# Performance work log

Measured on AMD Instinct MI355X. Metric: run time of the kernel, lower is better.

Reference implementation:

```python
import jax, jax.numpy as jnp
import numpy as np

B, F, D, L, N = 2048, 40, 64, 3, 40  # batch, num_fields, embed_dim, num_layers, num_subspaces


def setup_inputs() -> dict:
    key = jax.random.key(0)
    inputs = jax.random.normal(key, (B, F, D), dtype=jnp.float32)
    # Parameters per layer, matching torch init exactly:
    #   W     = identity(D) repeated over out_subspaces -> [N, D, D]
    #   alpha = ones([num_fields, in_subspaces, out_subspaces]); in_subspaces == F for
    #           layer 0 and == N afterwards; with N == F all layers share shape [F, N, N]
    #   h     = ones([N, D, 1])
    W = jnp.broadcast_to(jnp.eye(D, dtype=jnp.float32), (L, N, D, D)).copy()
    alpha = jnp.ones((L, F, N, N), dtype=jnp.float32)
    h = jnp.ones((L, N, D, 1), dtype=jnp.float32)
    return {"inputs": inputs, "W": W, "alpha": alpha, "h": h}


def _fusion_layer(B0, Bi, W, alpha, h):
    # Original math: fusion[b,n,D,d] = sum_{f,i} alpha[f,i,n] * B0[b,f,D] * Bi[b,i,d]
    #                out[b,n,D]     = sum_d fusion[b,n,D,d] * W[n,D,d] * h[n,d]
    # Reordered to avoid the [b,f,n,D,d] outer-product tensor:
    M = W * h[:, :, 0][:, None, :]                 # [n, D, d] = W * h broadcast over D
    C = jnp.einsum('bid,nDd->binD', Bi, M)         # contract embed dim d first
    out = jnp.einsum('bfD,fin,binD->bnD', B0, alpha, C)
    return out


def reference(inputs, W, alpha, h):
    B_i = inputs
    for l in range(L):
        B_i = _fusion_layer(inputs, B_i, W[l], alpha[l], h[l])
    return B_i
```

## Files before the change

kernel.cpp:

```cpp
#include <hip/hip_runtime.h>


typedef __bf16 bf16x8 __attribute__((ext_vector_type(8)));
typedef float  f32x16 __attribute__((ext_vector_type(16)));
typedef unsigned short us4 __attribute__((ext_vector_type(4)));

constexpr int BATCH = 2048;
constexpr int FDIM  = 40;
constexpr int DDIM  = 64;
constexpr int LAY   = 3;
constexpr int IPAD  = 64;
constexpr int FPAD  = 48;
constexpr int NSPL  = 4;
constexpr int NPB   = FDIM / NSPL;

__device__ __forceinline__ unsigned short f2bf(float f) {
  union { float f; unsigned u; } v; v.f = f;
  unsigned r = v.u + 0x7fff + ((v.u >> 16) & 1);
  return (unsigned short)(r >> 16);
}

__global__ __launch_bounds__(256) void prep_all(
    const float* __restrict__ inputs, const float* __restrict__ W,
    const float* __restrict__ h, const float* __restrict__ alpha,
    unsigned short* __restrict__ B0b, unsigned short* __restrict__ B0T,
    unsigned short* __restrict__ M, unsigned short* __restrict__ AT) {
  __shared__ float lds[FDIM][DDIM + 1];
  if (blockIdx.x < BATCH) {
    const int b = blockIdx.x;
    const float* src = inputs + (size_t)b * FDIM * DDIM;
    for (int cch = threadIdx.x; cch < FDIM * DDIM / 4; cch += 256) {
      float4 v = reinterpret_cast<const float4*>(src)[cch];
      int e = cch * 4;
      int f = e >> 6, d = e & 63;
      lds[f][d] = v.x; lds[f][d + 1] = v.y; lds[f][d + 2] = v.z; lds[f][d + 3] = v.w;
      us4 o = { f2bf(v.x), f2bf(v.y), f2bf(v.z), f2bf(v.w) };
      reinterpret_cast<us4*>(B0b + (size_t)b * FDIM * DDIM)[cch] = o;
    }
    __syncthreads();
    for (int cch = threadIdx.x; cch < DDIM * FPAD / 4; cch += 256) {
      int f4 = cch % (FPAD / 4);
      int d  = cch / (FPAD / 4);
      us4 o = {0, 0, 0, 0};
      if (f4 < FDIM / 4) {
        int f = f4 * 4;
        o[0] = f2bf(lds[f][d]);     o[1] = f2bf(lds[f + 1][d]);
        o[2] = f2bf(lds[f + 2][d]); o[3] = f2bf(lds[f + 3][d]);
      }
      reinterpret_cast<us4*>(B0T + (size_t)b * DDIM * FPAD)[cch] = o;
    }
    return;
  }
  int j = (blockIdx.x - BATCH) * 256 + threadIdx.x;
  const int nM4 = LAY * FDIM * DDIM * DDIM / 4;
  const int nA4 = LAY * FDIM * IPAD * FPAD / 4;
  if (j < nM4) {
    int e  = j * 4;
    int d  = e & 63;
    int ln = e >> 12;
    float4 wv = *reinterpret_cast<const float4*>(W + e);
    float4 hv = *reinterpret_cast<const float4*>(h + ln * DDIM + d);
    us4 o = { f2bf(wv.x * hv.x), f2bf(wv.y * hv.y), f2bf(wv.z * hv.z), f2bf(wv.w * hv.w) };
    *reinterpret_cast<us4*>(M + e) = o;
    return;
  }
  j -= nM4;
  if (j >= nA4) return;
  {
    int e  = j * 4;
    int f  = e % FPAD;
    int ii = (e / FPAD) % IPAD;
    int n  = (e / (FPAD * IPAD)) % FDIM;
    int l  = e / (FPAD * IPAD * FDIM);
    us4 o = {0, 0, 0, 0};
    if (ii < FDIM) {
#pragma unroll
      for (int k = 0; k < 4; ++k)
        if (f + k < FDIM)
          o[k] = f2bf(alpha[(((size_t)l * FDIM + f + k) * FDIM + ii) * FDIM + n]);
    }
    *reinterpret_cast<us4*>(AT + e) = o;
  }
}

template <bool FINAL>
__global__ __launch_bounds__(128, 2) void layer_k(
    const unsigned short* __restrict__ Bi,
    const unsigned short* __restrict__ B0T,
    const unsigned short* __restrict__ Mt,
    const unsigned short* __restrict__ ATt,
    void* __restrict__ outp)
{
  const int tid  = threadIdx.x;
  const int lane = tid & 63;
  const int w    = tid >> 6;
  const int c    = lane & 31;
  const int h    = lane >> 5;
  const int bg   = blockIdx.x >> 2;
  const int nBase = (blockIdx.x & 3) * NPB;
  const int bb   = bg * 4 + w * 2;

  bf16x8 aBi[2][2][4];
#pragma unroll
  for (int b2 = 0; b2 < 2; ++b2)
#pragma unroll
    for (int it = 0; it < 2; ++it) {
      int row = it * 32 + c; if (row > FDIM - 1) row = FDIM - 1;
#pragma unroll
      for (int ks = 0; ks < 4; ++ks)
        aBi[b2][it][ks] = *reinterpret_cast<const bf16x8*>(
            Bi + ((size_t)(bb + b2) * FDIM + row) * DDIM + ks * 16 + h * 8);
    }

  bf16x8 bT[2][2][3];
#pragma unroll
  for (int b2 = 0; b2 < 2; ++b2)
#pragma unroll
    for (int dt = 0; dt < 2; ++dt)
#pragma unroll
      for (int ks = 0; ks < 3; ++ks)
        bT[b2][dt][ks] = *reinterpret_cast<const bf16x8*>(
            B0T + ((size_t)(bb + b2) * DDIM + dt * 32 + c) * FPAD + ks * 16 + h * 8);

  for (int ln = 0; ln < NPB; ++ln) {
    const int n = nBase + ln;
    const unsigned short* Mn = Mt  + n * (DDIM * DDIM);
    const unsigned short* An = ATt + n * (IPAD * FPAD);

    bf16x8 mb[2][4];
#pragma unroll
    for (int dt = 0; dt < 2; ++dt)
#pragma unroll
      for (int ks = 0; ks < 4; ++ks)
        mb[dt][ks] = *reinterpret_cast<const bf16x8*>(
            Mn + (dt * 32 + c) * DDIM + ks * 16 + h * 8);

    bf16x8 at[2][3];
#pragma unroll
    for (int it = 0; it < 2; ++it)
#pragma unroll
      for (int ks = 0; ks < 3; ++ks)
        at[it][ks] = *reinterpret_cast<const bf16x8*>(
            An + (it * 32 + c) * FPAD + ks * 16 + h * 8);

    float pout[2][2] = {{0.f, 0.f}, {0.f, 0.f}};

#pragma unroll
    for (int it = 0; it < 2; ++it) {
#pragma unroll
      for (int dt = 0; dt < 2; ++dt) {
        f32x16 aC0 = {0,0,0,0,0,0,0,0,0,0,0,0,0,0,0,0};
        f32x16 aC1 = {0,0,0,0,0,0,0,0,0,0,0,0,0,0,0,0};
        f32x16 aR0 = {0,0,0,0,0,0,0,0,0,0,0,0,0,0,0,0};
        f32x16 aR1 = {0,0,0,0,0,0,0,0,0,0,0,0,0,0,0,0};
        __builtin_amdgcn_s_setprio(1);
#pragma unroll
        for (int ks = 0; ks < 3; ++ks) {
          aC0 = __builtin_amdgcn_mfma_f32_32x32x16_bf16(aBi[0][it][ks], mb[dt][ks], aC0, 0, 0, 0);
          aC1 = __builtin_amdgcn_mfma_f32_32x32x16_bf16(aBi[1][it][ks], mb[dt][ks], aC1, 0, 0, 0);
          aR0 = __builtin_amdgcn_mfma_f32_32x32x16_bf16(at[it][ks], bT[0][dt][ks], aR0, 0, 0, 0);
          aR1 = __builtin_amdgcn_mfma_f32_32x32x16_bf16(at[it][ks], bT[1][dt][ks], aR1, 0, 0, 0);
        }
        aC0 = __builtin_amdgcn_mfma_f32_32x32x16_bf16(aBi[0][it][3], mb[dt][3], aC0, 0, 0, 0);
        aC1 = __builtin_amdgcn_mfma_f32_32x32x16_bf16(aBi[1][it][3], mb[dt][3], aC1, 0, 0, 0);
        __builtin_amdgcn_s_setprio(0);
        {
          float t0 = 0.f, t1 = 0.f, t2 = 0.f, t3 = 0.f;
#pragma unroll
          for (int r = 0; r < 4; ++r) {
            t0 += aC0[r] * aR0[r];         t1 += aC0[r + 4] * aR0[r + 4];
            t2 += aC0[r + 8] * aR0[r + 8]; t3 += aC0[r + 12] * aR0[r + 12];
          }
          pout[0][dt] += (t0 + t1) + (t2 + t3);
        }
        {
          float t0 = 0.f, t1 = 0.f, t2 = 0.f, t3 = 0.f;
#pragma unroll
          for (int r = 0; r < 4; ++r) {
            t0 += aC1[r] * aR1[r];         t1 += aC1[r + 4] * aR1[r + 4];
            t2 += aC1[r + 8] * aR1[r + 8]; t3 += aC1[r + 12] * aR1[r + 12];
          }
          pout[1][dt] += (t0 + t1) + (t2 + t3);
        }
      }
    }

#pragma unroll
    for (int b2 = 0; b2 < 2; ++b2) {
      float v0 = pout[b2][0] + __shfl_xor(pout[b2][0], 32, 64);
      float v1 = pout[b2][1] + __shfl_xor(pout[b2][1], 32, 64);
      float val = h ? v1 : v0;
      size_t off = ((size_t)(bb + b2) * FDIM + n) * DDIM + lane;
      if (FINAL) ((float*)outp)[off] = val;
      else       ((unsigned short*)outp)[off] = f2bf(val);
    }
  }
}

extern "C" void kernel_launch(void* const* d_in, const int* in_sizes, int n_in,
                              void* d_out, int out_size, void* d_ws, size_t ws_size,
                              hipStream_t stream) {
  const float* inputs = (const float*)d_in[0];
  const float* W      = (const float*)d_in[1];
  const float* alpha  = (const float*)d_in[2];
  const float* h      = (const float*)d_in[3];

  char* ws = (char*)d_ws;
  const size_t S   = (size_t)BATCH * FDIM * DDIM * 2;
  const size_t ST  = (size_t)BATCH * DDIM * FPAD * 2;
  unsigned short* Bi1 = (unsigned short*)(ws);
  unsigned short* Bi2 = (unsigned short*)(ws + S);
  unsigned short* B0b = (unsigned short*)(ws + 2 * S);
  unsigned short* B0T = (unsigned short*)(ws + 3 * S);
  unsigned short* Mb  = (unsigned short*)(ws + 3 * S + ST);
  unsigned short* ATb = (unsigned short*)(ws + 3 * S + ST + (size_t)LAY * FDIM * DDIM * DDIM * 2);

  const int nPrep4 = (LAY * FDIM * DDIM * DDIM + LAY * FDIM * IPAD * FPAD) / 4;
  const int prepBlocks = BATCH + (nPrep4 + 255) / 256;
  prep_all<<<prepBlocks, 256, 0, stream>>>(inputs, W, h, alpha, B0b, B0T, Mb, ATb);

  dim3 grid(BATCH / 4 * NSPL), blk(128);
  const size_t mL = (size_t)FDIM * DDIM * DDIM;
  const size_t aL = (size_t)FDIM * IPAD * FPAD;
  layer_k<false><<<grid, blk, 0, stream>>>(B0b, B0T, Mb, ATb, Bi1);
  layer_k<false><<<grid, blk, 0, stream>>>(Bi1, B0T, Mb + mL, ATb + aL, Bi2);
  layer_k<true ><<<grid, blk, 0, stream>>>(Bi2, B0T, Mb + 2 * mL, ATb + 2 * aL, d_out);
}
```

Measured before the change: 261.6 us.

## Stage per-subspace M and alpha tiles in LDS shared across 8 waves

Each block now has 512 threads and covers 16 batch rows instead of 4. The W*h and alpha tiles for each pair of subspaces are loaded cooperatively into double-buffered LDS, with an XOR swizzle on M, instead of every wave reading them from global memory. Staging the next chunk is interleaved with compute, and block indices are remapped so neighbouring subspace splits land together. The MFMA loop is also split per batch to lower register pressure. This adds a barrier per chunk and about 60KB of LDS per block, and the grid shrinks to 512 blocks, which may limit latency hiding.

```diff
diff --git a/kernel.cpp b/kernel.cpp
--- a/kernel.cpp
+++ b/kernel.cpp
@@ -13,6 +13,8 @@
 constexpr int FPAD  = 48;
 constexpr int NSPL  = 4;
 constexpr int NPB   = FDIM / NSPL;
+constexpr int BPB   = 16;
+constexpr int NCH   = NPB / 2;
 
 __device__ __forceinline__ unsigned short f2bf(float f) {
   union { float f; unsigned u; } v; v.f = f;
@@ -84,21 +86,27 @@
 }
 
 template <bool FINAL>
-__global__ __launch_bounds__(128, 2) void layer_k(
+__global__ __launch_bounds__(512, 2) void layer_k(
     const unsigned short* __restrict__ Bi,
     const unsigned short* __restrict__ B0T,
     const unsigned short* __restrict__ Mt,
     const unsigned short* __restrict__ ATt,
     void* __restrict__ outp)
 {
+  __shared__ unsigned short smM[2][2][64 * 64];
+  __shared__ unsigned short smA[2][2][64 * 56];
+
   const int tid  = threadIdx.x;
   const int lane = tid & 63;
   const int w    = tid >> 6;
   const int c    = lane & 31;
   const int h    = lane >> 5;
-  const int bg   = blockIdx.x >> 2;
-  const int nBase = (blockIdx.x & 3) * NPB;
-  const int bb   = bg * 4 + w * 2;
+
+  const int L  = (blockIdx.x & 7) * 64 + (blockIdx.x >> 3);
+  const int bg = L >> 2;
+  const int ns = L & 3;
+  const int nBase = ns * NPB;
+  const int bb = bg * BPB + w * 2;
 
   bf16x8 aBi[2][2][4];
 #pragma unroll
@@ -111,7 +119,6 @@
         aBi[b2][it][ks] = *reinterpret_cast<const bf16x8*>(
             Bi + ((size_t)(bb + b2) * FDIM + row) * DDIM + ks * 16 + h * 8);
     }
-
   bf16x8 bT[2][2][3];
 #pragma unroll
   for (int b2 = 0; b2 < 2; ++b2)
@@ -122,69 +129,93 @@
         bT[b2][dt][ks] = *reinterpret_cast<const bf16x8*>(
             B0T + ((size_t)(bb + b2) * DDIM + dt * 32 + c) * FPAD + ks * 16 + h * 8);
 
-  for (int ln = 0; ln < NPB; ++ln) {
-    const int n = nBase + ln;
-    const unsigned short* Mn = Mt  + n * (DDIM * DDIM);
-    const unsigned short* An = ATt + n * (IPAD * FPAD);
-
-    bf16x8 mb[2][4];
+  auto stageL = [&](int cc, bf16x8 (&sM)[2], bf16x8 (&sA)[2]) {
+#pragma unroll
+    for (int r = 0; r < 2; ++r) {
+      int k = tid + r * 512;
+      int nn = k >> 9, rem = k & 511;
+      int row = rem >> 3, c8 = rem & 7;
+      sM[r] = *reinterpret_cast<const bf16x8*>(
+          Mt + (size_t)(nBase + cc * 2 + nn) * (DDIM * DDIM) + row * 64 + c8 * 8);
+    }
+#pragma unroll
+    for (int r = 0; r < 2; ++r) {
+      int k = tid + r * 512;
+      if (k < 768) {
+        int nn = k / 384, rem = k % 384;
+        int row = rem / 6, c6 = rem % 6;
+        sA[r] = *reinterpret_cast<const bf16x8*>(
+            ATt + (size_t)(nBase + cc * 2 + nn) * (IPAD * FPAD) + row * 48 + c6 * 8);
+      }
+    }
+  };
+  auto stageW = [&](int cc, const bf16x8 (&sM)[2], const bf16x8 (&sA)[2]) {
+    int bs = cc & 1;
+#pragma unroll
+    for (int r = 0; r < 2; ++r) {
+      int k = tid + r * 512;
+      int nn = k >> 9, rem = k & 511;
+      int row = rem >> 3, c8 = rem & 7;
+      *reinterpret_cast<bf16x8*>(
+          &smM[bs][nn][row * 64 + ((c8 ^ (row & 7)) * 8)]) = sM[r];
+    }
+#pragma unroll
+    for (int r = 0; r < 2; ++r) {
+      int k = tid + r * 512;
+      if (k < 768) {
+        int nn = k / 384, rem = k % 384;
+        int row = rem / 6, c6 = rem % 6;
+        *reinterpret_cast<bf16x8*>(&smA[bs][nn][row * 56 + c6 * 8]) = sA[r];
+      }
+    }
+  };
+
+  auto compute = [&](int nl, int bs) {
+    const int n  = nBase + nl;
+    const int nn = nl & 1;
+    const unsigned short* mL = &smM[bs][nn][0];
+    const unsigned short* aL = &smA[bs][nn][0];
+    bf16x8 mb[2][4], at[2][3];
 #pragma unroll
     for (int dt = 0; dt < 2; ++dt)
 #pragma unroll
       for (int ks = 0; ks < 4; ++ks)
         mb[dt][ks] = *reinterpret_cast<const bf16x8*>(
-            Mn + (dt * 32 + c) * DDIM + ks * 16 + h * 8);
-
-    bf16x8 at[2][3];
+            mL + (dt * 32 + c) * 64 + (((ks * 2 + h) ^ (c & 7)) * 8));
 #pragma unroll
     for (int it = 0; it < 2; ++it)
 #pragma unroll
       for (int ks = 0; ks < 3; ++ks)
         at[it][ks] = *reinterpret_cast<const bf16x8*>(
-            An + (it * 32 + c) * FPAD + ks * 16 + h * 8);
+            aL + (it * 32 + c) * 56 + (ks * 2 + h) * 8);
 
     float pout[2][2] = {{0.f, 0.f}, {0.f, 0.f}};
-
 #pragma unroll
     for (int it = 0; it < 2; ++it) {
 #pragma unroll
       for (int dt = 0; dt < 2; ++dt) {
-        f32x16 aC0 = {0,0,0,0,0,0,0,0,0,0,0,0,0,0,0,0};
-        f32x16 aC1 = {0,0,0,0,0,0,0,0,0,0,0,0,0,0,0,0};
-        f32x16 aR0 = {0,0,0,0,0,0,0,0,0,0,0,0,0,0,0,0};
-        f32x16 aR1 = {0,0,0,0,0,0,0,0,0,0,0,0,0,0,0,0};
-        __builtin_amdgcn_s_setprio(1);
-#pragma unroll
-        for (int ks = 0; ks < 3; ++ks) {
-          aC0 = __builtin_amdgcn_mfma_f32_32x32x16_bf16(aBi[0][it][ks], mb[dt][ks], aC0, 0, 0, 0);
-          aC1 = __builtin_amdgcn_mfma_f32_32x32x16_bf16(aBi[1][it][ks], mb[dt][ks], aC1, 0, 0, 0);
-          aR0 = __builtin_amdgcn_mfma_f32_32x32x16_bf16(at[it][ks], bT[0][dt][ks], aR0, 0, 0, 0);
-          aR1 = __builtin_amdgcn_mfma_f32_32x32x16_bf16(at[it][ks], bT[1][dt][ks], aR1, 0, 0, 0);
+#pragma unroll
+        for (int b2 = 0; b2 < 2; ++b2) {
+          f32x16 aC = {0,0,0,0,0,0,0,0,0,0,0,0,0,0,0,0};
+          f32x16 aR = {0,0,0,0,0,0,0,0,0,0,0,0,0,0,0,0};
+          __builtin_amdgcn_s_setprio(1);
+#pragma unroll
+          for (int ks = 0; ks < 3; ++ks) {
+            aC = __builtin_amdgcn_mfma_f32_32x32x16_bf16(aBi[b2][it][ks], mb[dt][ks], aC, 0, 0, 0);
+            aR = __builtin_amdgcn_mfma_f32_32x32x16_bf16(at[it][ks], bT[b2][dt][ks], aR, 0, 0, 0);
+          }
+          aC = __builtin_amdgcn_mfma_f32_32x32x16_bf16(aBi[b2][it][3], mb[dt][3], aC, 0, 0, 0);
+          __builtin_amdgcn_s_setprio(0);
+          float t0 = 0.f, t1 = 0.f, t2 = 0.f, t3 = 0.f;
+#pragma unroll
+          for (int r = 0; r < 4; ++r) {
+            t0 += aC[r] * aR[r];         t1 += aC[r + 4] * aR[r + 4];
+            t2 += aC[r + 8] * aR[r + 8]; t3 += aC[r + 12] * aR[r + 12];
+          }
+          pout[b2][dt] += (t0 + t1) + (t2 + t3);
         }
-        aC0 = __builtin_amdgcn_mfma_f32_32x32x16_bf16(aBi[0][it][3], mb[dt][3], aC0, 0, 0, 0);
-        aC1 = __builtin_amdgcn_mfma_f32_32x32x16_bf16(aBi[1][it][3], mb[dt][3], aC1, 0, 0, 0);
-        __builtin_amdgcn_s_setprio(0);
-        {
-          float t0 = 0.f, t1 = 0.f, t2 = 0.f, t3 = 0.f;
-#pragma unroll
-          for (int r = 0; r < 4; ++r) {
-            t0 += aC0[r] * aR0[r];         t1 += aC0[r + 4] * aR0[r + 4];
-            t2 += aC0[r + 8] * aR0[r + 8]; t3 += aC0[r + 12] * aR0[r + 12];
-          }
-          pout[0][dt] += (t0 + t1) + (t2 + t3);
-        }
-        {
-          float t0 = 0.f, t1 = 0.f, t2 = 0.f, t3 = 0.f;
-#pragma unroll
-          for (int r = 0; r < 4; ++r) {
-            t0 += aC1[r] * aR1[r];         t1 += aC1[r + 4] * aR1[r + 4];
-            t2 += aC1[r + 8] * aR1[r + 8]; t3 += aC1[r + 12] * aR1[r + 12];
-          }
-          pout[1][dt] += (t0 + t1) + (t2 + t3);
-        }
-      }
-    }
-
+      }
+    }
 #pragma unroll
     for (int b2 = 0; b2 < 2; ++b2) {
       float v0 = pout[b2][0] + __shfl_xor(pout[b2][0], 32, 64);
@@ -194,6 +225,24 @@
       if (FINAL) ((float*)outp)[off] = val;
       else       ((unsigned short*)outp)[off] = f2bf(val);
     }
+  };
+
+  {
+    bf16x8 sM[2], sA[2];
+    stageL(0, sM, sA);
+    stageW(0, sM, sA);
+  }
+  __syncthreads();
+#pragma unroll 1
+  for (int cc = 0; cc < NCH; ++cc) {
+    const int bs = cc & 1;
+    const int nf = w & 1;
+    bf16x8 sM[2], sA[2];
+    if (cc + 1 < NCH) stageL(cc + 1, sM, sA);
+    compute(cc * 2 + nf, bs);
+    if (cc + 1 < NCH) stageW(cc + 1, sM, sA);
+    compute(cc * 2 + (nf ^ 1), bs);
+    __syncthreads();
   }
 }
 
@@ -219,7 +268,7 @@
   const int prepBlocks = BATCH + (nPrep4 + 255) / 256;
   prep_all<<<prepBlocks, 256, 0, stream>>>(inputs, W, h, alpha, B0b, B0T, Mb, ATb);
 
-  dim3 grid(BATCH / 4 * NSPL), blk(128);
+  dim3 grid(BATCH / BPB * NSPL), blk(512);
   const size_t mL = (size_t)FDIM * DDIM * DDIM;
   const size_t aL = (size_t)FDIM * IPAD * FPAD;
   layer_k<false><<<grid, blk, 0, stream>>>(B0b, B0T, Mb, ATb, Bi1);
```

After: 235.0 us. -10.2%, faster.

## Stage per-subspace M and alpha slabs in LDS via double-buffered async DMA

Applied to the files above, without the earlier changes.

Each per-n M and alpha-transpose slab is now loaded cooperatively into double-buffered shared memory with global_load_lds, so 4 waves (8 batch rows) share one load instead of each wave re-reading from global/L2. The M slab gets an XOR swizzle applied in prep to avoid LDS bank conflicts, the alpha slab uses a 56-element row pitch, the block grows to 256 threads, and the block index is remapped to group neighbouring blocks. The MFMA loop is also reordered to keep only two accumulators live at a time, cutting register pressure. In exchange there is a block-wide barrier per n and added LDS use, which may limit occupancy.

```diff
diff --git a/kernel.cpp b/kernel.cpp
--- a/kernel.cpp
+++ b/kernel.cpp
@@ -9,15 +9,24 @@
 constexpr int FDIM  = 40;
 constexpr int DDIM  = 64;
 constexpr int LAY   = 3;
-constexpr int IPAD  = 64;
 constexpr int FPAD  = 48;
+constexpr int APAD  = 56;
 constexpr int NSPL  = 4;
 constexpr int NPB   = FDIM / NSPL;
+constexpr int BPB   = 8;
+constexpr int MSLAB = DDIM * DDIM;
+constexpr int ASLAB = DDIM * APAD;
 
 __device__ __forceinline__ unsigned short f2bf(float f) {
   union { float f; unsigned u; } v; v.f = f;
   unsigned r = v.u + 0x7fff + ((v.u >> 16) & 1);
   return (unsigned short)(r >> 16);
+}
+
+__device__ __forceinline__ void dma16(unsigned short* lds, const unsigned short* g) {
+  __builtin_amdgcn_global_load_lds(
+      (const __attribute__((address_space(1))) unsigned int*)g,
+      (__attribute__((address_space(3))) unsigned int*)lds, 16, 0, 0);
 }
 
 __global__ __launch_bounds__(256) void prep_all(
@@ -52,26 +61,29 @@
     return;
   }
   int j = (blockIdx.x - BATCH) * 256 + threadIdx.x;
-  const int nM4 = LAY * FDIM * DDIM * DDIM / 4;
-  const int nA4 = LAY * FDIM * IPAD * FPAD / 4;
+  const int nM4 = LAY * FDIM * MSLAB / 4;
+  const int nA4 = LAY * FDIM * ASLAB / 4;
   if (j < nM4) {
-    int e  = j * 4;
-    int d  = e & 63;
-    int ln = e >> 12;
-    float4 wv = *reinterpret_cast<const float4*>(W + e);
-    float4 hv = *reinterpret_cast<const float4*>(h + ln * DDIM + d);
-    us4 o = { f2bf(wv.x * hv.x), f2bf(wv.y * hv.y), f2bf(wv.z * hv.z), f2bf(wv.w * hv.w) };
-    *reinterpret_cast<us4*>(M + e) = o;
+    int e   = j * 4;
+    int ln  = e >> 12;
+    int row = (e >> 6) & 63;
+    int jc  = (e >> 3) & 7;
+    int o   = e & 7;
+    int ds  = ((jc ^ (row & 7)) << 3) + o;
+    float4 wv = *reinterpret_cast<const float4*>(W + ((size_t)ln * 64 + row) * 64 + ds);
+    float4 hv = *reinterpret_cast<const float4*>(h + (size_t)ln * 64 + ds);
+    us4 ov = { f2bf(wv.x * hv.x), f2bf(wv.y * hv.y), f2bf(wv.z * hv.z), f2bf(wv.w * hv.w) };
+    *reinterpret_cast<us4*>(M + e) = ov;
     return;
   }
   j -= nM4;
   if (j >= nA4) return;
   {
     int e  = j * 4;
-    int f  = e % FPAD;
-    int ii = (e / FPAD) % IPAD;
-    int n  = (e / (FPAD * IPAD)) % FDIM;
-    int l  = e / (FPAD * IPAD * FDIM);
+    int f  = e % APAD;
+    int ii = (e / APAD) & 63;
+    int n  = (e / ASLAB) % FDIM;
+    int l  = e / (ASLAB * FDIM);
     us4 o = {0, 0, 0, 0};
     if (ii < FDIM) {
 #pragma unroll
@@ -84,21 +96,27 @@
 }
 
 template <bool FINAL>
-__global__ __launch_bounds__(128, 2) void layer_k(
+__global__ __launch_bounds__(256, 4) void layer_k(
     const unsigned short* __restrict__ Bi,
     const unsigned short* __restrict__ B0T,
     const unsigned short* __restrict__ Mt,
     const unsigned short* __restrict__ ATt,
     void* __restrict__ outp)
 {
+  __shared__ unsigned short smM[2][MSLAB];
+  __shared__ unsigned short smA[2][ASLAB];
+
   const int tid  = threadIdx.x;
   const int lane = tid & 63;
   const int w    = tid >> 6;
   const int c    = lane & 31;
   const int h    = lane >> 5;
-  const int bg   = blockIdx.x >> 2;
-  const int nBase = (blockIdx.x & 3) * NPB;
-  const int bb   = bg * 4 + w * 2;
+
+  const int L  = (blockIdx.x & 7) * 128 + (blockIdx.x >> 3);
+  const int bg = L >> 2;
+  const int ns = L & 3;
+  const int nBase = ns * NPB;
+  const int bb = bg * BPB + w * 2;
 
   bf16x8 aBi[2][2][4];
 #pragma unroll
@@ -111,7 +129,6 @@
         aBi[b2][it][ks] = *reinterpret_cast<const bf16x8*>(
             Bi + ((size_t)(bb + b2) * FDIM + row) * DDIM + ks * 16 + h * 8);
     }
-
   bf16x8 bT[2][2][3];
 #pragma unroll
   for (int b2 = 0; b2 < 2; ++b2)
@@ -122,69 +139,65 @@
         bT[b2][dt][ks] = *reinterpret_cast<const bf16x8*>(
             B0T + ((size_t)(bb + b2) * DDIM + dt * 32 + c) * FPAD + ks * 16 + h * 8);
 
-  for (int ln = 0; ln < NPB; ++ln) {
-    const int n = nBase + ln;
-    const unsigned short* Mn = Mt  + n * (DDIM * DDIM);
-    const unsigned short* An = ATt + n * (IPAD * FPAD);
-
-    bf16x8 mb[2][4];
+  const f32x16 z16 = {0,0,0,0,0,0,0,0,0,0,0,0,0,0,0,0};
+
+  auto dmaChunk = [&](int nl, int bs) {
+    const unsigned short* Ms = Mt  + (size_t)(nBase + nl) * MSLAB;
+    const unsigned short* As = ATt + (size_t)(nBase + nl) * ASLAB;
+#pragma unroll
+    for (int r = 0; r < 2; ++r) {
+      int k = tid + r * 256;
+      dma16(&smM[bs][k * 8], Ms + k * 8);
+    }
+    dma16(&smA[bs][tid * 8], As + tid * 8);
+    if (tid < 192) dma16(&smA[bs][(tid + 256) * 8], As + (tid + 256) * 8);
+  };
+
+  auto compute = [&](int nl, int bs) {
+    const int n = nBase + nl;
+    const unsigned short* mL = &smM[bs][0];
+    const unsigned short* aL = &smA[bs][0];
+    bf16x8 mb[2][4], at[2][3];
 #pragma unroll
     for (int dt = 0; dt < 2; ++dt)
 #pragma unroll
       for (int ks = 0; ks < 4; ++ks)
         mb[dt][ks] = *reinterpret_cast<const bf16x8*>(
-            Mn + (dt * 32 + c) * DDIM + ks * 16 + h * 8);
-
-    bf16x8 at[2][3];
+            mL + (dt * 32 + c) * 64 + (((ks * 2 + h) ^ (c & 7)) * 8));
 #pragma unroll
     for (int it = 0; it < 2; ++it)
 #pragma unroll
       for (int ks = 0; ks < 3; ++ks)
         at[it][ks] = *reinterpret_cast<const bf16x8*>(
-            An + (it * 32 + c) * FPAD + ks * 16 + h * 8);
+            aL + (it * 32 + c) * APAD + (ks * 2 + h) * 8);
 
     float pout[2][2] = {{0.f, 0.f}, {0.f, 0.f}};
-
 #pragma unroll
     for (int it = 0; it < 2; ++it) {
 #pragma unroll
       for (int dt = 0; dt < 2; ++dt) {
-        f32x16 aC0 = {0,0,0,0,0,0,0,0,0,0,0,0,0,0,0,0};
-        f32x16 aC1 = {0,0,0,0,0,0,0,0,0,0,0,0,0,0,0,0};
-        f32x16 aR0 = {0,0,0,0,0,0,0,0,0,0,0,0,0,0,0,0};
-        f32x16 aR1 = {0,0,0,0,0,0,0,0,0,0,0,0,0,0,0,0};
-        __builtin_amdgcn_s_setprio(1);
-#pragma unroll
-        for (int ks = 0; ks < 3; ++ks) {
-          aC0 = __builtin_amdgcn_mfma_f32_32x32x16_bf16(aBi[0][it][ks], mb[dt][ks], aC0, 0, 0, 0);
-          aC1 = __builtin_amdgcn_mfma_f32_32x32x16_bf16(aBi[1][it][ks], mb[dt][ks], aC1, 0, 0, 0);
-          aR0 = __builtin_amdgcn_mfma_f32_32x32x16_bf16(at[it][ks], bT[0][dt][ks], aR0, 0, 0, 0);
-          aR1 = __builtin_amdgcn_mfma_f32_32x32x16_bf16(at[it][ks], bT[1][dt][ks], aR1, 0, 0, 0);
-        }
-        aC0 = __builtin_amdgcn_mfma_f32_32x32x16_bf16(aBi[0][it][3], mb[dt][3], aC0, 0, 0, 0);
-        aC1 = __builtin_amdgcn_mfma_f32_32x32x16_bf16(aBi[1][it][3], mb[dt][3], aC1, 0, 0, 0);
-        __builtin_amdgcn_s_setprio(0);
-        {
+#pragma unroll
+        for (int b2 = 0; b2 < 2; ++b2) {
+          __builtin_amdgcn_s_setprio(1);
+          f32x16 aC = __builtin_amdgcn_mfma_f32_32x32x16_bf16(aBi[b2][it][0], mb[dt][0], z16, 0, 0, 0);
+          f32x16 aR = __builtin_amdgcn_mfma_f32_32x32x16_bf16(at[it][0], bT[b2][dt][0], z16, 0, 0, 0);
+#pragma unroll
+          for (int ks = 1; ks < 3; ++ks) {
+            aC = __builtin_amdgcn_mfma_f32_32x32x16_bf16(aBi[b2][it][ks], mb[dt][ks], aC, 0, 0, 0);
+            aR = __builtin_amdgcn_mfma_f32_32x32x16_bf16(at[it][ks], bT[b2][dt][ks], aR, 0, 0, 0);
+          }
+          aC = __builtin_amdgcn_mfma_f32_32x32x16_bf16(aBi[b2][it][3], mb[dt][3], aC, 0, 0, 0);
+          __builtin_amdgcn_s_setprio(0);
           float t0 = 0.f, t1 = 0.f, t2 = 0.f, t3 = 0.f;
 #pragma unroll
           for (int r = 0; r < 4; ++r) {
-            t0 += aC0[r] * aR0[r];         t1 += aC0[r + 4] * aR0[r + 4];
-            t2 += aC0[r + 8] * aR0[r + 8]; t3 += aC0[r + 12] * aR0[r + 12];
+            t0 += aC[r] * aR[r];         t1 += aC[r + 4] * aR[r + 4];
+            t2 += aC[r + 8] * aR[r + 8]; t3 += aC[r + 12] * aR[r + 12];
           }
-          pout[0][dt] += (t0 + t1) + (t2 + t3);
-        }
-        {
-          float t0 = 0.f, t1 = 0.f, t2 = 0.f, t3 = 0.f;
-#pragma unroll
-          for (int r = 0; r < 4; ++r) {
-            t0 += aC1[r] * aR1[r];         t1 += aC1[r + 4] * aR1[r + 4];
-            t2 += aC1[r + 8] * aR1[r + 8]; t3 += aC1[r + 12] * aR1[r + 12];
-          }
-          pout[1][dt] += (t0 + t1) + (t2 + t3);
+          pout[b2][dt] += (t0 + t1) + (t2 + t3);
         }
       }
     }
-
 #pragma unroll
     for (int b2 = 0; b2 < 2; ++b2) {
       float v0 = pout[b2][0] + __shfl_xor(pout[b2][0], 32, 64);
@@ -194,6 +207,16 @@
       if (FINAL) ((float*)outp)[off] = val;
       else       ((unsigned short*)outp)[off] = f2bf(val);
     }
+  };
+
+  dmaChunk(0, 0);
+  __syncthreads();
+#pragma unroll 1
+  for (int cc = 0; cc < NPB; ++cc) {
+    const int bs = cc & 1;
+    if (cc + 1 < NPB) dmaChunk(cc + 1, bs ^ 1);
+    compute(cc, bs);
+    __syncthreads();
   }
 }
 
@@ -213,15 +236,15 @@
   unsigned short* B0b = (unsigned short*)(ws + 2 * S);
   unsigned short* B0T = (unsigned short*)(ws + 3 * S);
   unsigned short* Mb  = (unsigned short*)(ws + 3 * S + ST);
-  unsigned short* ATb = (unsigned short*)(ws + 3 * S + ST + (size_t)LAY * FDIM * DDIM * DDIM * 2);
-
-  const int nPrep4 = (LAY * FDIM * DDIM * DDIM + LAY * FDIM * IPAD * FPAD) / 4;
+  unsigned short* ATb = (unsigned short*)(ws + 3 * S + ST + (size_t)LAY * FDIM * MSLAB * 2);
+
+  const int nPrep4 = (LAY * FDIM * MSLAB + LAY * FDIM * ASLAB) / 4;
   const int prepBlocks = BATCH + (nPrep4 + 255) / 256;
   prep_all<<<prepBlocks, 256, 0, stream>>>(inputs, W, h, alpha, B0b, B0T, Mb, ATb);
 
-  dim3 grid(BATCH / 4 * NSPL), blk(128);
-  const size_t mL = (size_t)FDIM * DDIM * DDIM;
-  const size_t aL = (size_t)FDIM * IPAD * FPAD;
+  dim3 grid(BATCH / BPB * NSPL), blk(256);
+  const size_t mL = (size_t)FDIM * MSLAB;
+  const size_t aL = (size_t)FDIM * ASLAB;
   layer_k<false><<<grid, blk, 0, stream>>>(B0b, B0T, Mb, ATb, Bi1);
   layer_k<false><<<grid, blk, 0, stream>>>(Bi1, B0T, Mb + mL, ATb + aL, Bi2);
   layer_k<true ><<<grid, blk, 0, stream>>>(Bi2, B0T, Mb + 2 * mL, ATb + 2 * aL, d_out);
```

Measured after the change: 908.6 us. 3.47x slower.
